# Kernel tuning notes

Hardware: AMD Instinct MI355X
Metric: run time of the kernel (lower is better)

## Reference

```python
import jax, jax.numpy as jnp
import numpy as np

N_NODES = 10000
N_EDGES = 640000
D = 128


def setup_inputs() -> dict:
    key = jax.random.key(0)
    k1, k2, k3, k4 = jax.random.split(key, 4)
    X = jax.random.normal(k1, (N_NODES, D), dtype=jnp.float32)
    Y = jax.random.normal(k2, (N_EDGES, D), dtype=jnp.float32)
    # nn.Linear(in, out, bias=False): weight shape (out, in), y = Y @ W.T
    W = jax.random.normal(k3, (D, D), dtype=jnp.float32) * (1.0 / np.sqrt(D))
    edge_index = jax.random.randint(k4, (N_EDGES, 2), 0, N_NODES, dtype=jnp.int64)
    return {"X": X, "Y": Y, "W": W, "edge_index": edge_index}


def reference(X, Y, W, edge_index):
    # Edge transform: (E, d_in) @ (d_in, d_out) -> (E, d_out)
    Y_prime = jnp.einsum('ei,oi->eo', Y, W)
    # Scatter-add transformed edge features to source nodes
    src = edge_index[:, 0]
    agg = jax.ops.segment_sum(Y_prime, src, num_segments=X.shape[0])  # (N, d_out)
    # Residual + activation
    X_prime = jax.nn.relu(X + agg)
    return (X_prime, Y_prime)
```

## Files before the change

kernel.cpp:

```cpp
#include <hip/hip_runtime.h>

#define N_NODES 10000
#define N_EDGES 640000
#define DD 128

typedef __attribute__((ext_vector_type(8))) short short8;
typedef __attribute__((ext_vector_type(8))) float f32x8;
typedef __attribute__((ext_vector_type(4))) float f32x4;
typedef __attribute__((ext_vector_type(2))) float f32x2;

__device__ __forceinline__ unsigned pack_bf2(float lo, float hi) {
  return __builtin_amdgcn_perm(__float_as_uint(hi), __float_as_uint(lo), 0x07060302u);
}

__device__ __forceinline__ void stage_w(const float* __restrict__ W,
                                        short8* lwr) {
  const int tid = threadIdx.x;
#pragma unroll
  for (int t = 0; t < 8; ++t) {
    int s = t * 256 + tid;
    f32x8 v = *(const f32x8*)(W + (size_t)s * 8);
    short8 av;
    unsigned* au = (unsigned*)&av;
    au[0] = pack_bf2(v[0], v[1]);
    au[1] = pack_bf2(v[2], v[3]);
    au[2] = pack_bf2(v[4], v[5]);
    au[3] = pack_bf2(v[6], v[7]);
    int j = s >> 4;
    int c = s & 15;
    lwr[(j << 4) | (c ^ (j & 7))] = av;
  }
  __syncthreads();
}

__global__ __launch_bounds__(256) void k_zero(int* __restrict__ count) {
  const int i = blockIdx.x * 256 + threadIdx.x;
  if (i < N_NODES) count[i] = 0;
}

__global__ __launch_bounds__(256) void k_hist(const int* __restrict__ EI,
                                              int* __restrict__ count) {
  const int e = blockIdx.x * 256 + threadIdx.x;
  atomicAdd(&count[EI[2 * e]], 1);
}

__global__ __launch_bounds__(1024) void k_scan(const int* __restrict__ count,
                                               int* __restrict__ rowptr,
                                               int* __restrict__ cursor) {
  __shared__ int part[1024];
  const int tid = threadIdx.x;
  const int base = tid * 10;
  int local[10];
  int s = 0;
#pragma unroll
  for (int i = 0; i < 10; ++i) {
    const int idx = base + i;
    const int v = (idx < N_NODES) ? count[idx] : 0;
    local[i] = s;
    s += v;
  }
  part[tid] = s;
  __syncthreads();
  for (int off = 1; off < 1024; off <<= 1) {
    int v = 0;
    if (tid >= off) v = part[tid - off];
    __syncthreads();
    if (tid >= off) part[tid] += v;
    __syncthreads();
  }
  const int excl = (tid > 0) ? part[tid - 1] : 0;
#pragma unroll
  for (int i = 0; i < 10; ++i) {
    const int idx = base + i;
    if (idx < N_NODES) {
      const int r = excl + local[i];
      rowptr[idx] = r;
      cursor[idx] = r;
    }
  }
  if (tid == 1023) rowptr[N_NODES] = part[1023];
}

__global__ __launch_bounds__(256) void k_fill(const int* __restrict__ EI,
                                              int* __restrict__ cursor,
                                              int* __restrict__ col) {
  const int e = blockIdx.x * 256 + threadIdx.x;
  const int s = EI[2 * e];
  const int pos = atomicAdd(&cursor[s], 1);
  col[pos] = e;
}

__global__ __launch_bounds__(256, 2) void k_gemm_big(
    const float* __restrict__ Y,
    const float* __restrict__ W,
    float* __restrict__ Yp) {
  __shared__ short8 lwr[2048];
  stage_w(W, lwr);
  const int wid  = threadIdx.x >> 6;
  const int lane = threadIdx.x & 63;
  const int l15  = lane & 15;
  const int lg   = lane >> 4;
  const int koff = lg * 8;
  const int ebase = blockIdx.x * 128 + wid * 32;

  short8 a[2][4];
#pragma unroll
  for (int mt = 0; mt < 2; ++mt) {
    const float* yr = Y + (size_t)(ebase + mt * 16 + l15) * DD;
#pragma unroll
    for (int kk = 0; kk < 4; ++kk) {
      f32x8 v = *(const f32x8*)(yr + kk * 32 + koff);
      short8 av;
      unsigned* au = (unsigned*)&av;
      au[0] = pack_bf2(v[0], v[1]);
      au[1] = pack_bf2(v[2], v[3]);
      au[2] = pack_bf2(v[4], v[5]);
      au[3] = pack_bf2(v[6], v[7]);
      a[mt][kk] = av;
    }
  }

  f32x4 acc[2][8];
#pragma unroll
  for (int mt = 0; mt < 2; ++mt)
#pragma unroll
    for (int nt = 0; nt < 8; ++nt)
      acc[mt][nt] = (f32x4){0.f, 0.f, 0.f, 0.f};

#pragma unroll
  for (int nt = 0; nt < 8; ++nt) {
    const int j = nt * 16 + l15;
#pragma unroll
    for (int kk = 0; kk < 4; ++kk) {
      const int kc = kk * 4 + lg;
      short8 b = lwr[(j << 4) | (kc ^ (j & 7))];
      acc[0][nt] = __builtin_amdgcn_mfma_f32_16x16x32_bf16(b, a[0][kk], acc[0][nt], 0, 0, 0);
      acc[1][nt] = __builtin_amdgcn_mfma_f32_16x16x32_bf16(b, a[1][kk], acc[1][nt], 0, 0, 0);
    }
  }

#pragma unroll
  for (int mt = 0; mt < 2; ++mt) {
    float* orow = Yp + (size_t)(ebase + mt * 16 + l15) * DD + lg * 4;
#pragma unroll
    for (int nt = 0; nt < 8; ++nt)
      __builtin_nontemporal_store(acc[mt][nt], (f32x4*)(orow + nt * 16));
  }
}

__global__ __launch_bounds__(256) void k_gather_y(
    const float* __restrict__ Y,
    const int* __restrict__ rowptr,
    const int* __restrict__ col,
    float* __restrict__ segY) {
  const int node = blockIdx.x * 4 + (threadIdx.x >> 6);
  const int lane = threadIdx.x & 63;
  const size_t co = 2 * lane;
  const int b  = rowptr[node];
  const int en = rowptr[node + 1];

  f32x2 acc = (f32x2){0.f, 0.f};
  int i = b;
  for (; i + 8 <= en; i += 8) {
    f32x2 v0 = *(const f32x2*)(Y + (size_t)col[i]     * DD + co);
    f32x2 v1 = *(const f32x2*)(Y + (size_t)col[i + 1] * DD + co);
    f32x2 v2 = *(const f32x2*)(Y + (size_t)col[i + 2] * DD + co);
    f32x2 v3 = *(const f32x2*)(Y + (size_t)col[i + 3] * DD + co);
    f32x2 v4 = *(const f32x2*)(Y + (size_t)col[i + 4] * DD + co);
    f32x2 v5 = *(const f32x2*)(Y + (size_t)col[i + 5] * DD + co);
    f32x2 v6 = *(const f32x2*)(Y + (size_t)col[i + 6] * DD + co);
    f32x2 v7 = *(const f32x2*)(Y + (size_t)col[i + 7] * DD + co);
    acc += v0; acc += v1; acc += v2; acc += v3;
    acc += v4; acc += v5; acc += v6; acc += v7;
  }
  for (; i < en; ++i) {
    acc += *(const f32x2*)(Y + (size_t)col[i] * DD + co);
  }
  *(f32x2*)(segY + (size_t)node * DD + co) = acc;
}

__global__ __launch_bounds__(256, 2) void k_small(
    const float* __restrict__ segY,
    const float* __restrict__ W,
    const float* __restrict__ X,
    float* __restrict__ Xp) {
  __shared__ short8 lwr[2048];
  stage_w(W, lwr);
  const int wid  = threadIdx.x >> 6;
  const int lane = threadIdx.x & 63;
  const int l15  = lane & 15;
  const int lg   = lane >> 4;
  const int koff = lg * 8;
  const int rbase = blockIdx.x * 128 + wid * 32;

  short8 a[2][4];
#pragma unroll
  for (int mt = 0; mt < 2; ++mt) {
    int row = rbase + mt * 16 + l15;
    if (row > N_NODES - 1) row = N_NODES - 1;
    const float* sr = segY + (size_t)row * DD + koff;
#pragma unroll
    for (int kk = 0; kk < 4; ++kk) {
      f32x8 v = *(const f32x8*)(sr + kk * 32);
      short8 av;
      unsigned* au = (unsigned*)&av;
      au[0] = pack_bf2(v[0], v[1]);
      au[1] = pack_bf2(v[2], v[3]);
      au[2] = pack_bf2(v[4], v[5]);
      au[3] = pack_bf2(v[6], v[7]);
      a[mt][kk] = av;
    }
  }

  f32x4 acc[2][8];
#pragma unroll
  for (int mt = 0; mt < 2; ++mt)
#pragma unroll
    for (int nt = 0; nt < 8; ++nt)
      acc[mt][nt] = (f32x4){0.f, 0.f, 0.f, 0.f};

#pragma unroll
  for (int nt = 0; nt < 8; ++nt) {
    const int j = nt * 16 + l15;
#pragma unroll
    for (int kk = 0; kk < 4; ++kk) {
      const int kc = kk * 4 + lg;
      short8 b = lwr[(j << 4) | (kc ^ (j & 7))];
      acc[0][nt] = __builtin_amdgcn_mfma_f32_16x16x32_bf16(b, a[0][kk], acc[0][nt], 0, 0, 0);
      acc[1][nt] = __builtin_amdgcn_mfma_f32_16x16x32_bf16(b, a[1][kk], acc[1][nt], 0, 0, 0);
    }
  }

#pragma unroll
  for (int mt = 0; mt < 2; ++mt) {
    const int row = rbase + mt * 16 + l15;
    if (row < N_NODES) {
      const float* xr = X  + (size_t)row * DD + lg * 4;
      float*       orow = Xp + (size_t)row * DD + lg * 4;
#pragma unroll
      for (int nt = 0; nt < 8; ++nt) {
        f32x4 x = *(const f32x4*)(xr + nt * 16);
        f32x4 v = acc[mt][nt] + x;
        f32x4 r;
        r[0] = v[0] > 0.f ? v[0] : 0.f;
        r[1] = v[1] > 0.f ? v[1] : 0.f;
        r[2] = v[2] > 0.f ? v[2] : 0.f;
        r[3] = v[3] > 0.f ? v[3] : 0.f;
        *(f32x4*)(orow + nt * 16) = r;
      }
    }
  }
}

extern "C" void kernel_launch(void* const* d_in, const int* in_sizes, int n_in,
                              void* d_out, int out_size, void* d_ws, size_t ws_size,
                              hipStream_t stream) {
  const float* X  = (const float*)d_in[0];
  const float* Y  = (const float*)d_in[1];
  const float* W  = (const float*)d_in[2];
  const int*   EI = (const int*)d_in[3];

  float* Xp = (float*)d_out;
  float* Yp = Xp + (size_t)N_NODES * DD;

  int* w      = (int*)d_ws;
  int* count  = w;
  int* rowptr = w + 10000;
  int* cursor = w + 20001;
  int* col    = w + 30001;
  float* segY = (float*)(w + 670001 + 15);

  k_zero<<<(N_NODES + 255) / 256, 256, 0, stream>>>(count);
  k_hist<<<N_EDGES / 256, 256, 0, stream>>>(EI, count);
  k_scan<<<1, 1024, 0, stream>>>(count, rowptr, cursor);
  k_fill<<<N_EDGES / 256, 256, 0, stream>>>(EI, cursor, col);
  k_gemm_big<<<N_EDGES / 128, 256, 0, stream>>>(Y, W, Yp);
  k_gather_y<<<N_NODES / 4, 256, 0, stream>>>(Y, rowptr, col, segY);
  k_small<<<(N_NODES + 127) / 128, 256, 0, stream>>>(segY, W, X, Xp);
}
```

Before: 314.7 us.

## Make edge GEMM persistent with register prefetch of next Y chunk

The edge GEMM kernel now launches a fixed grid of 512 blocks that loop over 128-row chunks. Each block stages W into LDS only once, and it prefetches the next chunk's Y rows into registers while the MFMAs and stores for the current chunk run. This removes repeated W staging across 5000 blocks and overlaps global loads with compute. In exchange it uses more registers, which may lower occupancy, and the fixed grid may not load-balance well across CUs.

```diff
diff --git a/kernel.cpp b/kernel.cpp
--- a/kernel.cpp
+++ b/kernel.cpp
@@ -3,6 +3,8 @@
 #define N_NODES 10000
 #define N_EDGES 640000
 #define DD 128
+#define N_CHUNKS (N_EDGES / 128)
+#define GEMM_GRID 512
 
 typedef __attribute__((ext_vector_type(8))) short short8;
 typedef __attribute__((ext_vector_type(8))) float f32x8;
@@ -101,50 +103,86 @@
   const int l15  = lane & 15;
   const int lg   = lane >> 4;
   const int koff = lg * 8;
-  const int ebase = blockIdx.x * 128 + wid * 32;
-
-  short8 a[2][4];
-#pragma unroll
-  for (int mt = 0; mt < 2; ++mt) {
-    const float* yr = Y + (size_t)(ebase + mt * 16 + l15) * DD;
+
+  f32x4 raw[16];
+  int c = blockIdx.x;
+
+  {
+    const int ebase = c * 128 + wid * 32;
+    const float* p0 = Y + (size_t)(ebase + l15) * DD + koff;
+    const float* p1 = Y + (size_t)(ebase + 16 + l15) * DD + koff;
 #pragma unroll
     for (int kk = 0; kk < 4; ++kk) {
-      f32x8 v = *(const f32x8*)(yr + kk * 32 + koff);
-      short8 av;
-      unsigned* au = (unsigned*)&av;
-      au[0] = pack_bf2(v[0], v[1]);
-      au[1] = pack_bf2(v[2], v[3]);
-      au[2] = pack_bf2(v[4], v[5]);
-      au[3] = pack_bf2(v[6], v[7]);
-      a[mt][kk] = av;
-    }
-  }
-
-  f32x4 acc[2][8];
-#pragma unroll
-  for (int mt = 0; mt < 2; ++mt)
-#pragma unroll
-    for (int nt = 0; nt < 8; ++nt)
-      acc[mt][nt] = (f32x4){0.f, 0.f, 0.f, 0.f};
-
-#pragma unroll
-  for (int nt = 0; nt < 8; ++nt) {
-    const int j = nt * 16 + l15;
-#pragma unroll
-    for (int kk = 0; kk < 4; ++kk) {
-      const int kc = kk * 4 + lg;
-      short8 b = lwr[(j << 4) | (kc ^ (j & 7))];
-      acc[0][nt] = __builtin_amdgcn_mfma_f32_16x16x32_bf16(b, a[0][kk], acc[0][nt], 0, 0, 0);
-      acc[1][nt] = __builtin_amdgcn_mfma_f32_16x16x32_bf16(b, a[1][kk], acc[1][nt], 0, 0, 0);
-    }
-  }
-
-#pragma unroll
-  for (int mt = 0; mt < 2; ++mt) {
-    float* orow = Yp + (size_t)(ebase + mt * 16 + l15) * DD + lg * 4;
-#pragma unroll
-    for (int nt = 0; nt < 8; ++nt)
-      __builtin_nontemporal_store(acc[mt][nt], (f32x4*)(orow + nt * 16));
+      raw[kk * 2 + 0]     = *(const f32x4*)(p0 + kk * 32);
+      raw[kk * 2 + 1]     = *(const f32x4*)(p0 + kk * 32 + 4);
+      raw[8 + kk * 2 + 0] = *(const f32x4*)(p1 + kk * 32);
+      raw[8 + kk * 2 + 1] = *(const f32x4*)(p1 + kk * 32 + 4);
+    }
+  }
+
+#pragma unroll 1
+  while (true) {
+    const int ebase = c * 128 + wid * 32;
+    const int cn = c + GEMM_GRID;
+
+    short8 a[2][4];
+#pragma unroll
+    for (int mt = 0; mt < 2; ++mt)
+#pragma unroll
+      for (int kk = 0; kk < 4; ++kk) {
+        f32x4 v0 = raw[mt * 8 + kk * 2];
+        f32x4 v1 = raw[mt * 8 + kk * 2 + 1];
+        short8 av;
+        unsigned* au = (unsigned*)&av;
+        au[0] = pack_bf2(v0[0], v0[1]);
+        au[1] = pack_bf2(v0[2], v0[3]);
+        au[2] = pack_bf2(v1[0], v1[1]);
+        au[3] = pack_bf2(v1[2], v1[3]);
+        a[mt][kk] = av;
+      }
+
+    if (cn < N_CHUNKS) {
+      const int eb2 = cn * 128 + wid * 32;
+      const float* p0 = Y + (size_t)(eb2 + l15) * DD + koff;
+      const float* p1 = Y + (size_t)(eb2 + 16 + l15) * DD + koff;
+#pragma unroll
+      for (int kk = 0; kk < 4; ++kk) {
+        raw[kk * 2 + 0]     = *(const f32x4*)(p0 + kk * 32);
+        raw[kk * 2 + 1]     = *(const f32x4*)(p0 + kk * 32 + 4);
+        raw[8 + kk * 2 + 0] = *(const f32x4*)(p1 + kk * 32);
+        raw[8 + kk * 2 + 1] = *(const f32x4*)(p1 + kk * 32 + 4);
+      }
+    }
+
+    f32x4 acc[2][8];
+#pragma unroll
+    for (int mt = 0; mt < 2; ++mt)
+#pragma unroll
+      for (int nt = 0; nt < 8; ++nt)
+        acc[mt][nt] = (f32x4){0.f, 0.f, 0.f, 0.f};
+
+#pragma unroll
+    for (int nt = 0; nt < 8; ++nt) {
+      const int j = nt * 16 + l15;
+#pragma unroll
+      for (int kk = 0; kk < 4; ++kk) {
+        const int kc = kk * 4 + lg;
+        short8 b = lwr[(j << 4) | (kc ^ (j & 7))];
+        acc[0][nt] = __builtin_amdgcn_mfma_f32_16x16x32_bf16(b, a[0][kk], acc[0][nt], 0, 0, 0);
+        acc[1][nt] = __builtin_amdgcn_mfma_f32_16x16x32_bf16(b, a[1][kk], acc[1][nt], 0, 0, 0);
+      }
+    }
+
+#pragma unroll
+    for (int mt = 0; mt < 2; ++mt) {
+      float* orow = Yp + (size_t)(ebase + mt * 16 + l15) * DD + lg * 4;
+#pragma unroll
+      for (int nt = 0; nt < 8; ++nt)
+        __builtin_nontemporal_store(acc[mt][nt], (f32x4*)(orow + nt * 16));
+    }
+
+    if (cn >= N_CHUNKS) break;
+    c = cn;
   }
 }
 
@@ -235,7 +273,7 @@
   for (int mt = 0; mt < 2; ++mt) {
     const int row = rbase + mt * 16 + l15;
     if (row < N_NODES) {
-      const float* xr = X  + (size_t)row * DD + lg * 4;
+      const float* xr   = X  + (size_t)row * DD + lg * 4;
       float*       orow = Xp + (size_t)row * DD + lg * 4;
 #pragma unroll
       for (int nt = 0; nt < 8; ++nt) {
@@ -274,7 +312,7 @@
   k_hist<<<N_EDGES / 256, 256, 0, stream>>>(EI, count);
   k_scan<<<1, 1024, 0, stream>>>(count, rowptr, cursor);
   k_fill<<<N_EDGES / 256, 256, 0, stream>>>(EI, cursor, col);
-  k_gemm_big<<<N_EDGES / 128, 256, 0, stream>>>(Y, W, Yp);
+  k_gemm_big<<<GEMM_GRID, 256, 0, stream>>>(Y, W, Yp);
   k_gather_y<<<N_NODES / 4, 256, 0, stream>>>(Y, rowptr, col, segY);
   k_small<<<(N_NODES + 127) / 128, 256, 0, stream>>>(segY, W, X, Xp);
 }
```

New measurement: 338.8 us. 1.08x slower.
